# Performance work log

Measured on AMD Instinct MI355X. Metric: run time of the kernel, lower is better.

The kernel has to match this reference:

```python
import jax, jax.numpy as jnp
import numpy as np

B, R, C, D = 8, 64, 16, 128  # batch, num_rows(taxa), patch_num, embed_dim


def _linear_init(key, fan_in, fan_out):
    lim = 1.0 / np.sqrt(fan_in)
    kw, kb = jax.random.split(key)
    W = jax.random.uniform(kw, (fan_in, fan_out), jnp.float32, -lim, lim)
    b = jax.random.uniform(kb, (fan_out,), jnp.float32, -lim, lim)
    return W, b


def setup_inputs() -> dict:
    key = jax.random.key(0)
    ks = jax.random.split(key, 8)
    row_np, col_np = np.triu_indices(R, k=1)  # n = R*(R-1)/2 = 2016 pairs
    hW, hb = _linear_init(ks[1], D, D)
    gW, gb = _linear_init(ks[2], D, D)
    qW, qb = _linear_init(ks[3], D, D)
    kW, kb = _linear_init(ks[4], D, D)
    s1W, s1b = _linear_init(ks[5], D, D)
    s2W, s2b = _linear_init(ks[6], D, 1)
    return {
        "batch_input": jax.random.normal(ks[0], (B, R, C, D), jnp.float32),
        "seq_mask": jnp.ones((B, 1, C), jnp.float32),
        "row": jnp.asarray(row_np, jnp.int32),
        "col": jnp.asarray(col_np, jnp.int32),
        "hW": hW, "hb": hb, "gW": gW, "gb": gb,
        "qW": qW, "qb": qb, "kW": kW, "kb": kb,
        "s1W": s1W, "s1b": s1b, "s2W": s2W, "s2b": s2b,
    }


def reference(batch_input, seq_mask, row, col,
              hW, hb, gW, gb, qW, qb, kW, kb, s1W, s1b, s2W, s2b):
    b, r, c, d = batch_input.shape
    n = row.shape[0]
    # pairwise gather: x_i, x_j -> [b, n, c, d]
    x_i = batch_input[:, row]
    x_j = batch_input[:, col]
    # sigmoid gate fusion of the pair
    h = (x_i - x_j) @ hW + hb
    z = jax.nn.sigmoid(h)
    x = z * x_i + (1.0 - z) * x_j
    # masked global attention over the batch_input 'memory' (r > 2 branch)
    q = x @ qW + qb                    # [b, n, c, d]
    k = batch_input @ kW + kb          # [b, r, c, d]
    scale = 1.0 / np.sqrt(d * c).astype(np.float32)
    alpha = jnp.einsum('bncd,brcd->bnr', q, k) * scale
    # -inf at (pair n, rows row[n] and col[n]); equivalent to += -inf on finite scores
    neg_mask = (jnp.zeros((n, r), bool)
                .at[jnp.arange(n), row].set(True)
                .at[jnp.arange(n), col].set(True))
    alpha = jnp.where(neg_mask[None], -jnp.inf, alpha)
    alpha = jax.nn.softmax(alpha, axis=-1)
    x_glob = jnp.einsum('bnr,brcd->bncd', alpha, batch_input)
    g = x_glob @ gW + gb
    w = jax.nn.sigmoid(g)
    x = (1.0 - w) * x + w * x_glob
    # s_out: Linear -> GELU(exact) -> Linear(d,1), then mask and reduce over c
    s = jax.nn.gelu(x @ s1W + s1b, approximate=False) @ s2W + s2b  # [b, n, c, 1]
    scores = s[..., 0] * seq_mask       # seq_mask [b,1,c] broadcasts over n
    return scores.sum(-1)               # [b, n]
```

## Files before the change

kernel.cpp:

```cpp
#include <hip/hip_runtime.h>
#include <hip/hip_bf16.h>
#include <math.h>

#define B_    8
#define R_    64
#define C_    16
#define D_    128
#define NPAIR 2016
#define CD    2048
#define PG    16
#define NPG   126
#define XSTR  136
#define LSTR  68
#define NEG_BIG (-1e30f)
#define SCALE 0.022097086912079608f

typedef __attribute__((ext_vector_type(8))) short short8;
typedef __attribute__((ext_vector_type(4))) float float4v;

#define WMH  0u
#define WML  16384u
#define WSH  98304u
#define VECO 131072u
#define QBKO 131592u
#define MO   132616u
#define XTO  1181192u
#define GTO  2229768u
#define HO   3278344u

__device__ __forceinline__ unsigned short f2b(float f){
    union { float f; unsigned int u; } v; v.f = f;
    const unsigned int r = v.u + 0x7FFFu + ((v.u >> 16) & 1u);
    return (unsigned short)(r >> 16);
}
__device__ __forceinline__ float b2f(unsigned short u){
    union { unsigned int i; float f; } v; v.i = ((unsigned int)u) << 16; return v.f;
}
__device__ __forceinline__ float lo2f(unsigned int u){
    union { unsigned int i; float f; } v; v.i = u << 16; return v.f;
}
__device__ __forceinline__ float hif2f(unsigned int u){
    union { unsigned int i; float f; } v; v.i = u & 0xffff0000u; return v.f;
}
__device__ __forceinline__ unsigned int pack2(float a, float b){
    unsigned int r;
    asm("v_cvt_pk_bf16_f32 %0, %1, %2" : "=v"(r) : "v"(a), "v"(b));
    return r;
}
__device__ __forceinline__ unsigned short f2b1(float a){
    unsigned int r;
    asm("v_cvt_pk_bf16_f32 %0, %1, %1" : "=v"(r) : "v"(a));
    return (unsigned short)r;
}
__device__ __forceinline__ void split_bf(float v, float* hi, float* lo){
    union { float f; unsigned int u; } x; x.f = v;
    const unsigned int r = (x.u + 0x7FFFu + ((x.u >> 16) & 1u)) & 0xffff0000u;
    union { unsigned int u; float f; } h; h.u = r;
    *hi = h.f; *lo = v - h.f;
}
__device__ __forceinline__ void splitw(float v, short* h, short* l){
    union { float f; unsigned int u; } x; x.f = v;
    const unsigned int rh = (x.u + 0x7FFFu + ((x.u >> 16) & 1u)) & 0xffff0000u;
    union { unsigned int u; float f; } hf; hf.u = rh;
    *h = (short)(rh >> 16);
    *l = (short)f2b(v - hf.f);
}
__device__ __forceinline__ float sigmoid_safe(float x){
    return __builtin_amdgcn_rcpf(1.f + __expf(-x));
}
__device__ __forceinline__ float gelu_tanh(float x){
    const float u = x*x;
    const float g2 = x*(1.5957691216057308f + 0.07135481627159f*u);
    return x * sigmoid_safe(g2);
}

__global__ __launch_bounds__(256) void k_prepA(
    const float* __restrict__ qW, const float* __restrict__ qb,
    const float* __restrict__ kW, const float* __restrict__ kb,
    unsigned short* __restrict__ ws)
{
    const int bid = blockIdx.x, t = threadIdx.x;
    if (bid < 64){
        __shared__ float sKW[2][128];
        const int e0 = bid*2;
        sKW[t>>7][t&127] = kW[(e0 + (t>>7))*128 + (t&127)];
        __syncthreads();
        const int e = t>>7, d = t&127;
        const float* qr = qW + d*128;
        const float* kr = sKW[e];
        float acc = 0.f;
        #pragma unroll 8
        for (int g = 0; g < 128; g += 4){
            const float4 qv = *reinterpret_cast<const float4*>(qr + g);
            acc += qv.x*kr[g] + qv.y*kr[g+1] + qv.z*kr[g+2] + qv.w*kr[g+3];
        }
        float hi, lo; split_bf(acc, &hi, &lo);
        ws[WMH + d*128 + (e0+e)] = f2b(hi);
        ws[WML + d*128 + (e0+e)] = f2b(lo);
    } else {
        float* vec = (float*)(ws + VECO);
        if (t < 128){
            float a1 = 0.f, a2 = 0.f;
            #pragma unroll 8
            for (int g = 0; g < 128; g += 4){
                const float4 q4 = *reinterpret_cast<const float4*>(qW + t*128 + g);
                const float4 k4 = *reinterpret_cast<const float4*>(kW + t*128 + g);
                const float4 kb4 = *reinterpret_cast<const float4*>(kb + g);
                const float4 qb4 = *reinterpret_cast<const float4*>(qb + g);
                a1 += q4.x*kb4.x + q4.y*kb4.y + q4.z*kb4.z + q4.w*kb4.w;
                a2 += k4.x*qb4.x + k4.y*qb4.y + k4.z*qb4.z + k4.w*qb4.w;
            }
            vec[t] = a1;
            vec[128 + t] = a2;
        } else if (t == 128){
            float a = 0.f;
            for (int g = 0; g < 128; ++g) a = fmaf(qb[g], kb[g], a);
            vec[256] = a;
        }
    }
}

__global__ __launch_bounds__(512) void k_prepB(const float* __restrict__ x,
        const float* __restrict__ hW, const float* __restrict__ gW,
        const float* __restrict__ gb, const float* __restrict__ s1W,
        unsigned short* __restrict__ ws)
{
    __shared__ __align__(16) unsigned short smem[8832];
    __shared__ float sQ[4];
    const int bid = blockIdx.x, t = threadIdx.x;
    const int w = t >> 6, lane = t & 63, l15 = lane & 15, quad = lane >> 4;

    if (bid < 256){
        const bool isM = (bid >= 128);
        unsigned short* sH = smem;
        const int br0 = (bid & 127) * 4;
        const float* kqf = (const float*)(ws + VECO) + 128;
        const float* mbf = (const float*)(ws + VECO);
        if (t < 4) sQ[t] = 0.f;
        __syncthreads();
        float qacc[4] = {0.f, 0.f, 0.f, 0.f};
        #pragma unroll
        for (int i = 0; i < 4; ++i){
            const int flat = (t + 512*i)*4;
            const int lr = i;
            const int cd = flat & 2047;
            const float4 v = *reinterpret_cast<const float4*>(x + (size_t)(br0+lr)*CD + cd);
            const int ad = (lr*16 + (cd>>7))*XSTR + lr*8 + (cd & 127);
            uint2 uh;
            uh.x = pack2(v.x, v.y); uh.y = pack2(v.z, v.w);
            *reinterpret_cast<uint2*>(sH + ad) = uh;
            if (isM){
                const float4 kq4 = *reinterpret_cast<const float4*>(kqf + (cd & 127));
                qacc[i] = v.x*kq4.x + v.y*kq4.y + v.z*kq4.z + v.w*kq4.w;
            }
        }
        if (isM){
            #pragma unroll
            for (int i = 0; i < 4; ++i){
                float s = qacc[i];
                #pragma unroll
                for (int off = 1; off < 64; off <<= 1) s += __shfl_xor(s, off);
                if (lane == 0) atomicAdd(&sQ[i], s);
            }
        }
        __syncthreads();
        if (isM){
            const float bv = mbf[w*16 + l15];
            float4v acc[4];
            #pragma unroll
            for (int mt = 0; mt < 4; ++mt){ float4v d = {bv,bv,bv,bv}; acc[mt] = d; }
            #pragma unroll
            for (int ks = 0; ks < 4; ++ks){
                const int ko = ks*32 + quad*8;
                const int bd = (w*16 + l15)*128 + ko;
                const short8 bh = *reinterpret_cast<const short8*>(ws + WMH + bd);
                const short8 bl = *reinterpret_cast<const short8*>(ws + WML + bd);
                #pragma unroll
                for (int mt = 0; mt < 4; ++mt){
                    const int ad = (mt*16 + l15)*XSTR + mt*8 + ko;
                    const short8 ah = *reinterpret_cast<const short8*>(sH + ad);
                    float4v d = acc[mt];
                    d = __builtin_amdgcn_mfma_f32_16x16x32_bf16(ah, bh, d, 0,0,0);
                    d = __builtin_amdgcn_mfma_f32_16x16x32_bf16(ah, bl, d, 0,0,0);
                    acc[mt] = d;
                }
            }
            const int f = w*16 + l15;
            #pragma unroll
            for (int mt = 0; mt < 4; ++mt)
            #pragma unroll
            for (int e = 0; e < 4; ++e){
                const int c = quad*4 + e;
                ws[MO + (size_t)(br0+mt)*CD + c*128 + f] = f2b(acc[mt][e]);
            }
            if (t < 4){
                const float s0 = ((const float*)(ws + VECO))[256];
                ((float*)(ws + QBKO))[br0 + t] = sQ[t] + 16.f*s0;
            }
        } else {
            const int n = w*16 + l15;
            float4v acc[4];
            #pragma unroll
            for (int mt = 0; mt < 4; ++mt){ float4v z = {0.f,0.f,0.f,0.f}; acc[mt] = z; }
            #pragma unroll
            for (int ks = 0; ks < 4; ++ks){
                const int ko = ks*32 + quad*8;
                short8 bh, bl;
                #pragma unroll
                for (int j = 0; j < 8; ++j){
                    short hh, ll;
                    splitw(hW[(size_t)(ko+j)*128 + n], &hh, &ll);
                    bh[j] = hh; bl[j] = ll;
                }
                #pragma unroll
                for (int mt = 0; mt < 4; ++mt){
                    const int ad = (mt*16 + l15)*XSTR + mt*8 + ko;
                    const short8 ah = *reinterpret_cast<const short8*>(sH + ad);
                    float4v d = acc[mt];
                    d = __builtin_amdgcn_mfma_f32_16x16x32_bf16(ah, bh, d, 0,0,0);
                    d = __builtin_amdgcn_mfma_f32_16x16x32_bf16(ah, bl, d, 0,0,0);
                    acc[mt] = d;
                }
            }
            #pragma unroll
            for (int mt = 0; mt < 4; ++mt)
            #pragma unroll
            for (int e = 0; e < 4; ++e){
                const int c = quad*4 + e;
                ws[HO + (size_t)(br0+mt)*CD + c*128 + n] = f2b(acc[mt][e]);
            }
        }
    } else if (bid < 384){
        unsigned short* tileB = smem;
        const int gidx = bid - 256;
        const int b = gidx >> 4, cd0 = (gidx & 15)*128;
        #pragma unroll
        for (int i = 0; i < 16; ++i){
            const int idx = i*512 + t;
            const int r = idx >> 7, dd = idx & 127;
            tileB[r*138 + dd] = f2b(x[(size_t)(b*64 + r)*CD + cd0 + dd]);
        }
        __syncthreads();
        const int fA = w*16 + l15;
        float4v acc[4];
        #pragma unroll
        for (int nt = 0; nt < 4; ++nt){ float4v z = {0.f,0.f,0.f,0.f}; acc[nt] = z; }
        #pragma unroll
        for (int ks = 0; ks < 4; ++ks){
            const int ko = ks*32 + quad*8;
            short8 ah, al;
            #pragma unroll
            for (int j = 0; j < 8; ++j){
                short hh, ll;
                splitw(gW[(size_t)(ko+j)*128 + fA], &hh, &ll);
                ah[j] = hh; al[j] = ll;
            }
            #pragma unroll
            for (int nt = 0; nt < 4; ++nt){
                const short8 bb = *reinterpret_cast<const short8*>(tileB + (nt*16 + l15)*138 + ko);
                float4v d = acc[nt];
                d = __builtin_amdgcn_mfma_f32_16x16x32_bf16(ah, bb, d, 0,0,0);
                d = __builtin_amdgcn_mfma_f32_16x16x32_bf16(al, bb, d, 0,0,0);
                acc[nt] = d;
            }
        }
        #pragma unroll
        for (int nt = 0; nt < 4; ++nt)
        #pragma unroll
        for (int e = 0; e < 4; ++e){
            const int f = w*16 + quad*4 + e;
            const float val = acc[nt][e] + gb[f];
            ws[GTO + (size_t)(b*2048 + cd0 + f)*64 + nt*16 + l15] = f2b(val);
        }
    } else if (bid < 388){
        const int gid = (bid - 384)*4096 + t;
        #pragma unroll
        for (int i = 0; i < 8; ++i){
            const int g = gid + i*512;
            const int n = g >> 7, k = g & 127;
            ws[WSH + g] = f2b(s1W[k*128 + n]);
        }
    } else {
        unsigned short* tile = smem;
        const int blk = bid - 388;
        const int b = blk >> 4, cd0 = (blk & 15)*128;
        #pragma unroll
        for (int i = 0; i < 16; ++i){
            const int idx = i*512 + t;
            const int r = idx >> 7, cc = idx & 127;
            tile[cc*69 + r] = f2b(x[((size_t)(b*64 + r))*CD + cd0 + cc]);
        }
        __syncthreads();
        const unsigned int base = XTO + (unsigned int)(b*2048 + cd0)*64;
        #pragma unroll
        for (int j = 0; j < 16; ++j){
            const int idx = j*512 + t;
            const int cc = idx >> 6, r = idx & 63;
            ws[base + cc*64 + r] = tile[cc*69 + r];
        }
    }
}

__global__ __launch_bounds__(512, 4) void k_main(
    const float* __restrict__ x, const float* __restrict__ seq_mask,
    const int* __restrict__ row, const int* __restrict__ col,
    const float* __restrict__ hb, const float* __restrict__ s1b,
    const float* __restrict__ s2W, const float* __restrict__ s2b,
    const unsigned short* __restrict__ ws, float* __restrict__ out)
{
    __shared__ __align__(16) unsigned short sX[256*XSTR + 128];
    __shared__ __align__(16) unsigned short sAl[16*72];
    __shared__ float sLog[16*LSTR];
    __shared__ float sOut[PG];
    __shared__ float sMask[16];
    __shared__ int srp[PG], scp[PG];

    const int t = threadIdx.x;
    const int w = t >> 6, lane = t & 63, l15 = lane & 15, quad = lane >> 4;
    const int b = blockIdx.x, p0 = blockIdx.y * PG;
    const float* xb = x + (size_t)b * R_ * CD;
    const unsigned short* Hb = ws + HO + (size_t)b * R_ * CD;

    if (t < PG){ srp[t] = row[p0+t]; scp[t] = col[p0+t]; sOut[t] = 0.f; }
    if (t >= 32 && t < 48) sMask[t-32] = seq_mask[b*C_ + (t-32)];
    for (int i = t; i < 1152; i += 512) sAl[i] = 0;
    for (int i = t; i < 16*LSTR; i += 512) sLog[i] = 0.f;
    __syncthreads();

    #pragma unroll 4
    for (int i = 0; i < 16; ++i){
        const int flat = (t + 512*i)*4;
        const int p = flat >> 11, cd = flat & 2047;
        const int ri = srp[p], ci = scp[p];
        const float4 xi = *reinterpret_cast<const float4*>(xb + (size_t)ri*CD + cd);
        const float4 xj = *reinterpret_cast<const float4*>(xb + (size_t)ci*CD + cd);
        const uint2 Hi2 = *reinterpret_cast<const uint2*>(Hb + (size_t)ri*CD + cd);
        const uint2 Hj2 = *reinterpret_cast<const uint2*>(Hb + (size_t)ci*CD + cd);
        const float4 h4 = *reinterpret_cast<const float4*>(hb + (cd & 127));
        const float z0 = sigmoid_safe(lo2f(Hi2.x)  - lo2f(Hj2.x)  + h4.x);
        const float z1 = sigmoid_safe(hif2f(Hi2.x) - hif2f(Hj2.x) + h4.y);
        const float z2 = sigmoid_safe(lo2f(Hi2.y)  - lo2f(Hj2.y)  + h4.z);
        const float z3 = sigmoid_safe(hif2f(Hi2.y) - hif2f(Hj2.y) + h4.w);
        const float v0 = xj.x + z0*(xi.x - xj.x);
        const float v1 = xj.y + z1*(xi.y - xj.y);
        const float v2 = xj.z + z2*(xi.z - xj.z);
        const float v3 = xj.w + z3*(xi.w - xj.w);
        const int ad = (p*16 + (cd>>7))*XSTR + p*8 + (cd & 127);
        uint2 uv; uv.x = pack2(v0,v1); uv.y = pack2(v2,v3);
        *reinterpret_cast<uint2*>(sX + ad) = uv;
    }
    __syncthreads();

    {
        const int rt = w & 3, kh = w >> 2;
        const int r = rt*16 + l15;
        const unsigned short* Mr = ws + MO + ((size_t)b*64 + r)*CD + kh*1024;
        float4v d0 = {0.f,0.f,0.f,0.f}, d1 = {0.f,0.f,0.f,0.f};
        float4v d2 = {0.f,0.f,0.f,0.f}, d3 = {0.f,0.f,0.f,0.f};
        #pragma unroll
        for (int h = 0; h < 4; ++h){
            short8 bhr[8];
            #pragma unroll
            for (int u = 0; u < 8; ++u)
                bhr[u] = *reinterpret_cast<const short8*>(Mr + (h*8+u)*32 + quad*8);
            #pragma unroll
            for (int u = 0; u < 8; ++u){
                const int k = kh*1024 + (h*8+u)*32 + quad*8;
                const short8 ah = *reinterpret_cast<const short8*>(
                    sX + (l15*16 + (k>>7))*XSTR + l15*8 + (k & 127));
                if ((u&3) == 0)      d0 = __builtin_amdgcn_mfma_f32_16x16x32_bf16(ah, bhr[u], d0, 0,0,0);
                else if ((u&3) == 1) d1 = __builtin_amdgcn_mfma_f32_16x16x32_bf16(ah, bhr[u], d1, 0,0,0);
                else if ((u&3) == 2) d2 = __builtin_amdgcn_mfma_f32_16x16x32_bf16(ah, bhr[u], d2, 0,0,0);
                else                 d3 = __builtin_amdgcn_mfma_f32_16x16x32_bf16(ah, bhr[u], d3, 0,0,0);
            }
        }
        const float4v d = (d0 + d1) + (d2 + d3);
        #pragma unroll
        for (int e = 0; e < 4; ++e){
            const int pp = quad*4 + e;
            atomicAdd(&sLog[pp*LSTR + r], d[e]);
        }
    }
    __syncthreads();

    const unsigned short* XTb = ws + XTO + (size_t)b * CD * 64;
    const unsigned short* GTb = ws + GTO + (size_t)b * CD * 64;
    short8 px0[2], px1[2], pg0[2], pg1[2];
    #pragma unroll
    for (int j = 0; j < 2; ++j){
        const int cd = w*256 + j*16 + l15;
        px0[j] = *reinterpret_cast<const short8*>(XTb + (size_t)cd*64 + quad*8);
        px1[j] = *reinterpret_cast<const short8*>(XTb + (size_t)cd*64 + 32 + quad*8);
        pg0[j] = *reinterpret_cast<const short8*>(GTb + (size_t)cd*64 + quad*8);
        pg1[j] = *reinterpret_cast<const short8*>(GTb + (size_t)cd*64 + 32 + quad*8);
    }

    if (t < 256){
        const int pp = t >> 4, l = t & 15;
        const int ri = srp[pp], ci = scp[pp];
        const float* qbk = (const float*)(ws + QBKO);
        float v[4]; float m = NEG_BIG;
        #pragma unroll
        for (int k = 0; k < 4; ++k){
            const int r = l + 16*k;
            float lv = (sLog[pp*LSTR + r] + qbk[b*64 + r]) * SCALE;
            if (r == ri || r == ci) lv = NEG_BIG;
            v[k] = lv; m = fmaxf(m, lv);
        }
        #pragma unroll
        for (int s = 1; s < 16; s <<= 1) m = fmaxf(m, __shfl_xor(m, s));
        float e4[4]; float sum = 0.f;
        #pragma unroll
        for (int k = 0; k < 4; ++k){
            const int r = l + 16*k;
            const bool masked = (r == ri || r == ci);
            const float e = masked ? 0.f : __expf(fmaxf(v[k]-m, -80.f));
            e4[k] = e; sum += e;
        }
        #pragma unroll
        for (int s = 1; s < 16; s <<= 1) sum += __shfl_xor(sum, s);
        const float inv = __builtin_amdgcn_rcpf(sum);
        #pragma unroll
        for (int k = 0; k < 4; ++k) sAl[pp*72 + l + 16*k] = f2b1(e4[k]*inv);
    }
    __syncthreads();

    {
        const short8 Ah0 = *reinterpret_cast<const short8*>(sAl + l15*72 + quad*8);
        const short8 Ah1 = *reinterpret_cast<const short8*>(sAl + l15*72 + 32 + quad*8);
        #pragma unroll
        for (int j = 0; j < 16; ++j){
            const int s = j & 1;
            float4v dx = {0.f,0.f,0.f,0.f}, dg = {0.f,0.f,0.f,0.f};
            dx = __builtin_amdgcn_mfma_f32_16x16x32_bf16(Ah0, px0[s], dx, 0,0,0);
            dx = __builtin_amdgcn_mfma_f32_16x16x32_bf16(Ah1, px1[s], dx, 0,0,0);
            dg = __builtin_amdgcn_mfma_f32_16x16x32_bf16(Ah0, pg0[s], dg, 0,0,0);
            dg = __builtin_amdgcn_mfma_f32_16x16x32_bf16(Ah1, pg1[s], dg, 0,0,0);
            if (j + 2 < 16){
                const int cd2 = w*256 + (j+2)*16 + l15;
                px0[s] = *reinterpret_cast<const short8*>(XTb + (size_t)cd2*64 + quad*8);
                px1[s] = *reinterpret_cast<const short8*>(XTb + (size_t)cd2*64 + 32 + quad*8);
                pg0[s] = *reinterpret_cast<const short8*>(GTb + (size_t)cd2*64 + quad*8);
                pg1[s] = *reinterpret_cast<const short8*>(GTb + (size_t)cd2*64 + 32 + quad*8);
            }
            const int cd = w*256 + j*16 + l15;
            #pragma unroll
            for (int e = 0; e < 4; ++e){
                const int pp = quad*4 + e;
                const int ad = (pp*16 + (cd>>7))*XSTR + pp*8 + (cd & 127);
                const float wv = sigmoid_safe(dg[e]);
                const float xo = b2f(sX[ad]);
                sX[ad] = f2b1((1.f - wv)*xo + wv*dx[e]);
            }
        }
    }
    __syncthreads();

    {
        float4v acc16[16];
        const float bv = s1b[w*16 + l15];
        #pragma unroll
        for (int mt = 0; mt < 16; ++mt){ float4v d = {bv,bv,bv,bv}; acc16[mt] = d; }
        short8 bh4[4];
        #pragma unroll
        for (int ks = 0; ks < 4; ++ks)
            bh4[ks] = *reinterpret_cast<const short8*>(ws + WSH + (w*16 + l15)*128 + ks*32 + quad*8);
        #pragma unroll
        for (int ks = 0; ks < 4; ++ks){
            const int ko = ks*32 + quad*8;
            #pragma unroll
            for (int mt = 0; mt < 16; ++mt){
                const short8 a = *reinterpret_cast<const short8*>(sX + (mt*16 + l15)*XSTR + mt*8 + ko);
                acc16[mt] = __builtin_amdgcn_mfma_f32_16x16x32_bf16(a, bh4[ks], acc16[mt], 0,0,0);
            }
        }
        const float s2v = s2W[w*16 + l15];
        const float mk0 = sMask[quad*4+0], mk1 = sMask[quad*4+1];
        const float mk2 = sMask[quad*4+2], mk3 = sMask[quad*4+3];
        float psum[16];
        #pragma unroll
        for (int mt = 0; mt < 16; ++mt){
            float s = gelu_tanh(acc16[mt][0]) * mk0;
            s += gelu_tanh(acc16[mt][1]) * mk1;
            s += gelu_tanh(acc16[mt][2]) * mk2;
            s += gelu_tanh(acc16[mt][3]) * mk3;
            psum[mt] = s * s2v;
        }
        #pragma unroll
        for (int s = 1; s < 64; s <<= 1)
            #pragma unroll
            for (int mt = 0; mt < 16; ++mt) psum[mt] += __shfl_xor(psum[mt], s);
        if (lane == 0){
            #pragma unroll
            for (int mt = 0; mt < 16; ++mt) atomicAdd(&sOut[mt], psum[mt]);
        }
    }
    __syncthreads();

    if (t < PG){
        float msum = 0.f;
        #pragma unroll
        for (int c = 0; c < 16; ++c) msum += sMask[c];
        out[(size_t)b*NPAIR + p0 + t] = sOut[t] + s2b[0]*msum;
    }
}

extern "C" void kernel_launch(void* const* d_in, const int* in_sizes, int n_in,
                              void* d_out, int out_size, void* d_ws, size_t ws_size,
                              hipStream_t stream)
{
    const float* x    = (const float*)d_in[0];
    const float* mask = (const float*)d_in[1];
    const int*   row  = (const int*)d_in[2];
    const int*   col  = (const int*)d_in[3];
    const float* hW  = (const float*)d_in[4];  const float* hb  = (const float*)d_in[5];
    const float* gW  = (const float*)d_in[6];  const float* gb  = (const float*)d_in[7];
    const float* qW  = (const float*)d_in[8];  const float* qb  = (const float*)d_in[9];
    const float* kW  = (const float*)d_in[10]; const float* kb  = (const float*)d_in[11];
    const float* s1W = (const float*)d_in[12]; const float* s1b = (const float*)d_in[13];
    const float* s2W = (const float*)d_in[14]; const float* s2b = (const float*)d_in[15];

    unsigned short* ws = (unsigned short*)d_ws;

    k_prepA<<<65, 256, 0, stream>>>(qW, qb, kW, kb, ws);
    k_prepB<<<516, 512, 0, stream>>>(x, hW, gW, gb, s1W, ws);
    k_main<<<dim3(B_, NPG), 512, 0, stream>>>(x, mask, row, col,
                                              hb, s1b, s2W, s2b,
                                              ws, (float*)d_out);
}
```

Measured before the change: 227.3 us.

## Process 32 pairs per block with 1024 threads to reuse weight tiles

Doubles the pair group per block from 16 to 32 and the block size from 512 to 1024 threads, halving the grid. In the logits and global-attention stages each wave now runs two pair tiles against the same loaded M, XT and GT fragments. This cuts redundant global loads of those per-batch tiles per pair. The final s1 GEMM splits waves into two pair halves. In exchange the LDS footprint roughly doubles, so only one block fits per CU. The 1024-thread launch bound also tightens the register budget and risks spills.

```diff
diff --git a/kernel.cpp b/kernel.cpp
--- a/kernel.cpp
+++ b/kernel.cpp
@@ -8,8 +8,8 @@
 #define D_    128
 #define NPAIR 2016
 #define CD    2048
-#define PG    16
-#define NPG   126
+#define PG    32
+#define NPG   63
 #define XSTR  136
 #define LSTR  68
 #define NEG_BIG (-1e30f)
@@ -301,16 +301,16 @@
     }
 }
 
-__global__ __launch_bounds__(512, 4) void k_main(
+__global__ __launch_bounds__(1024, 4) void k_main(
     const float* __restrict__ x, const float* __restrict__ seq_mask,
     const int* __restrict__ row, const int* __restrict__ col,
     const float* __restrict__ hb, const float* __restrict__ s1b,
     const float* __restrict__ s2W, const float* __restrict__ s2b,
     const unsigned short* __restrict__ ws, float* __restrict__ out)
 {
-    __shared__ __align__(16) unsigned short sX[256*XSTR + 128];
-    __shared__ __align__(16) unsigned short sAl[16*72];
-    __shared__ float sLog[16*LSTR];
+    __shared__ __align__(16) unsigned short sX[512*XSTR + 256];
+    __shared__ __align__(16) unsigned short sAl[32*72];
+    __shared__ float sLog[32*LSTR];
     __shared__ float sOut[PG];
     __shared__ float sMask[16];
     __shared__ int srp[PG], scp[PG];
@@ -323,13 +323,13 @@
 
     if (t < PG){ srp[t] = row[p0+t]; scp[t] = col[p0+t]; sOut[t] = 0.f; }
     if (t >= 32 && t < 48) sMask[t-32] = seq_mask[b*C_ + (t-32)];
-    for (int i = t; i < 1152; i += 512) sAl[i] = 0;
-    for (int i = t; i < 16*LSTR; i += 512) sLog[i] = 0.f;
+    for (int i = t; i < 32*72; i += 1024) sAl[i] = 0;
+    for (int i = t; i < 32*LSTR; i += 1024) sLog[i] = 0.f;
     __syncthreads();
 
     #pragma unroll 4
     for (int i = 0; i < 16; ++i){
-        const int flat = (t + 512*i)*4;
+        const int flat = (t + 1024*i)*4;
         const int p = flat >> 11, cd = flat & 2047;
         const int ri = srp[p], ci = scp[p];
         const float4 xi = *reinterpret_cast<const float4*>(xb + (size_t)ri*CD + cd);
@@ -354,31 +354,40 @@
     {
         const int rt = w & 3, kh = w >> 2;
         const int r = rt*16 + l15;
-        const unsigned short* Mr = ws + MO + ((size_t)b*64 + r)*CD + kh*1024;
-        float4v d0 = {0.f,0.f,0.f,0.f}, d1 = {0.f,0.f,0.f,0.f};
-        float4v d2 = {0.f,0.f,0.f,0.f}, d3 = {0.f,0.f,0.f,0.f};
-        #pragma unroll
-        for (int h = 0; h < 4; ++h){
+        const unsigned short* Mr = ws + MO + ((size_t)b*64 + r)*CD + kh*512;
+        float4v d0a = {0.f,0.f,0.f,0.f}, d0b = {0.f,0.f,0.f,0.f};
+        float4v d1a = {0.f,0.f,0.f,0.f}, d1b = {0.f,0.f,0.f,0.f};
+        #pragma unroll
+        for (int h = 0; h < 2; ++h){
             short8 bhr[8];
             #pragma unroll
             for (int u = 0; u < 8; ++u)
                 bhr[u] = *reinterpret_cast<const short8*>(Mr + (h*8+u)*32 + quad*8);
             #pragma unroll
             for (int u = 0; u < 8; ++u){
-                const int k = kh*1024 + (h*8+u)*32 + quad*8;
-                const short8 ah = *reinterpret_cast<const short8*>(
-                    sX + (l15*16 + (k>>7))*XSTR + l15*8 + (k & 127));
-                if ((u&3) == 0)      d0 = __builtin_amdgcn_mfma_f32_16x16x32_bf16(ah, bhr[u], d0, 0,0,0);
-                else if ((u&3) == 1) d1 = __builtin_amdgcn_mfma_f32_16x16x32_bf16(ah, bhr[u], d1, 0,0,0);
-                else if ((u&3) == 2) d2 = __builtin_amdgcn_mfma_f32_16x16x32_bf16(ah, bhr[u], d2, 0,0,0);
-                else                 d3 = __builtin_amdgcn_mfma_f32_16x16x32_bf16(ah, bhr[u], d3, 0,0,0);
-            }
-        }
-        const float4v d = (d0 + d1) + (d2 + d3);
+                const int k = kh*512 + (h*8+u)*32 + quad*8;
+                const int khi = k >> 7, klo = k & 127;
+                const int pA = l15, pB = 16 + l15;
+                const short8 ahA = *reinterpret_cast<const short8*>(
+                    sX + (pA*16 + khi)*XSTR + pA*8 + klo);
+                const short8 ahB = *reinterpret_cast<const short8*>(
+                    sX + (pB*16 + khi)*XSTR + pB*8 + klo);
+                if (u & 1){
+                    d0b = __builtin_amdgcn_mfma_f32_16x16x32_bf16(ahA, bhr[u], d0b, 0,0,0);
+                    d1b = __builtin_amdgcn_mfma_f32_16x16x32_bf16(ahB, bhr[u], d1b, 0,0,0);
+                } else {
+                    d0a = __builtin_amdgcn_mfma_f32_16x16x32_bf16(ahA, bhr[u], d0a, 0,0,0);
+                    d1a = __builtin_amdgcn_mfma_f32_16x16x32_bf16(ahB, bhr[u], d1a, 0,0,0);
+                }
+            }
+        }
+        const float4v dA = d0a + d0b;
+        const float4v dB = d1a + d1b;
         #pragma unroll
         for (int e = 0; e < 4; ++e){
             const int pp = quad*4 + e;
-            atomicAdd(&sLog[pp*LSTR + r], d[e]);
+            atomicAdd(&sLog[pp*LSTR + r], dA[e]);
+            atomicAdd(&sLog[(16+pp)*LSTR + r], dB[e]);
         }
     }
     __syncthreads();
@@ -388,14 +397,14 @@
     short8 px0[2], px1[2], pg0[2], pg1[2];
     #pragma unroll
     for (int j = 0; j < 2; ++j){
-        const int cd = w*256 + j*16 + l15;
+        const int cd = w*128 + j*16 + l15;
         px0[j] = *reinterpret_cast<const short8*>(XTb + (size_t)cd*64 + quad*8);
         px1[j] = *reinterpret_cast<const short8*>(XTb + (size_t)cd*64 + 32 + quad*8);
         pg0[j] = *reinterpret_cast<const short8*>(GTb + (size_t)cd*64 + quad*8);
         pg1[j] = *reinterpret_cast<const short8*>(GTb + (size_t)cd*64 + 32 + quad*8);
     }
 
-    if (t < 256){
+    if (t < 512){
         const int pp = t >> 4, l = t & 15;
         const int ri = srp[pp], ci = scp[pp];
         const float* qbk = (const float*)(ws + QBKO);
@@ -426,55 +435,70 @@
     __syncthreads();
 
     {
-        const short8 Ah0 = *reinterpret_cast<const short8*>(sAl + l15*72 + quad*8);
-        const short8 Ah1 = *reinterpret_cast<const short8*>(sAl + l15*72 + 32 + quad*8);
-        #pragma unroll
-        for (int j = 0; j < 16; ++j){
+        const short8 AhA0 = *reinterpret_cast<const short8*>(sAl + l15*72 + quad*8);
+        const short8 AhA1 = *reinterpret_cast<const short8*>(sAl + l15*72 + 32 + quad*8);
+        const short8 AhB0 = *reinterpret_cast<const short8*>(sAl + (16+l15)*72 + quad*8);
+        const short8 AhB1 = *reinterpret_cast<const short8*>(sAl + (16+l15)*72 + 32 + quad*8);
+        #pragma unroll
+        for (int j = 0; j < 8; ++j){
             const int s = j & 1;
-            float4v dx = {0.f,0.f,0.f,0.f}, dg = {0.f,0.f,0.f,0.f};
-            dx = __builtin_amdgcn_mfma_f32_16x16x32_bf16(Ah0, px0[s], dx, 0,0,0);
-            dx = __builtin_amdgcn_mfma_f32_16x16x32_bf16(Ah1, px1[s], dx, 0,0,0);
-            dg = __builtin_amdgcn_mfma_f32_16x16x32_bf16(Ah0, pg0[s], dg, 0,0,0);
-            dg = __builtin_amdgcn_mfma_f32_16x16x32_bf16(Ah1, pg1[s], dg, 0,0,0);
-            if (j + 2 < 16){
-                const int cd2 = w*256 + (j+2)*16 + l15;
+            float4v dxA = {0.f,0.f,0.f,0.f}, dgA = {0.f,0.f,0.f,0.f};
+            float4v dxB = {0.f,0.f,0.f,0.f}, dgB = {0.f,0.f,0.f,0.f};
+            dxA = __builtin_amdgcn_mfma_f32_16x16x32_bf16(AhA0, px0[s], dxA, 0,0,0);
+            dxA = __builtin_amdgcn_mfma_f32_16x16x32_bf16(AhA1, px1[s], dxA, 0,0,0);
+            dgA = __builtin_amdgcn_mfma_f32_16x16x32_bf16(AhA0, pg0[s], dgA, 0,0,0);
+            dgA = __builtin_amdgcn_mfma_f32_16x16x32_bf16(AhA1, pg1[s], dgA, 0,0,0);
+            dxB = __builtin_amdgcn_mfma_f32_16x16x32_bf16(AhB0, px0[s], dxB, 0,0,0);
+            dxB = __builtin_amdgcn_mfma_f32_16x16x32_bf16(AhB1, px1[s], dxB, 0,0,0);
+            dgB = __builtin_amdgcn_mfma_f32_16x16x32_bf16(AhB0, pg0[s], dgB, 0,0,0);
+            dgB = __builtin_amdgcn_mfma_f32_16x16x32_bf16(AhB1, pg1[s], dgB, 0,0,0);
+            if (j + 2 < 8){
+                const int cd2 = w*128 + (j+2)*16 + l15;
                 px0[s] = *reinterpret_cast<const short8*>(XTb + (size_t)cd2*64 + quad*8);
                 px1[s] = *reinterpret_cast<const short8*>(XTb + (size_t)cd2*64 + 32 + quad*8);
                 pg0[s] = *reinterpret_cast<const short8*>(GTb + (size_t)cd2*64 + quad*8);
                 pg1[s] = *reinterpret_cast<const short8*>(GTb + (size_t)cd2*64 + 32 + quad*8);
             }
-            const int cd = w*256 + j*16 + l15;
+            const int cd = w*128 + j*16 + l15;
+            const int khi = cd >> 7, klo = cd & 127;
             #pragma unroll
             for (int e = 0; e < 4; ++e){
-                const int pp = quad*4 + e;
-                const int ad = (pp*16 + (cd>>7))*XSTR + pp*8 + (cd & 127);
-                const float wv = sigmoid_safe(dg[e]);
-                const float xo = b2f(sX[ad]);
-                sX[ad] = f2b1((1.f - wv)*xo + wv*dx[e]);
+                const int ppA = quad*4 + e;
+                const int adA = (ppA*16 + khi)*XSTR + ppA*8 + klo;
+                const float wvA = sigmoid_safe(dgA[e]);
+                const float xoA = b2f(sX[adA]);
+                sX[adA] = f2b1((1.f - wvA)*xoA + wvA*dxA[e]);
+                const int ppB = 16 + quad*4 + e;
+                const int adB = (ppB*16 + khi)*XSTR + ppB*8 + klo;
+                const float wvB = sigmoid_safe(dgB[e]);
+                const float xoB = b2f(sX[adB]);
+                sX[adB] = f2b1((1.f - wvB)*xoB + wvB*dxB[e]);
             }
         }
     }
     __syncthreads();
 
     {
+        const int mh = w >> 3, nw = w & 7;
         float4v acc16[16];
-        const float bv = s1b[w*16 + l15];
+        const float bv = s1b[nw*16 + l15];
         #pragma unroll
         for (int mt = 0; mt < 16; ++mt){ float4v d = {bv,bv,bv,bv}; acc16[mt] = d; }
         short8 bh4[4];
         #pragma unroll
         for (int ks = 0; ks < 4; ++ks)
-            bh4[ks] = *reinterpret_cast<const short8*>(ws + WSH + (w*16 + l15)*128 + ks*32 + quad*8);
+            bh4[ks] = *reinterpret_cast<const short8*>(ws + WSH + (nw*16 + l15)*128 + ks*32 + quad*8);
         #pragma unroll
         for (int ks = 0; ks < 4; ++ks){
             const int ko = ks*32 + quad*8;
             #pragma unroll
             for (int mt = 0; mt < 16; ++mt){
-                const short8 a = *reinterpret_cast<const short8*>(sX + (mt*16 + l15)*XSTR + mt*8 + ko);
+                const int p = mh*16 + mt;
+                const short8 a = *reinterpret_cast<const short8*>(sX + (p*16 + l15)*XSTR + p*8 + ko);
                 acc16[mt] = __builtin_amdgcn_mfma_f32_16x16x32_bf16(a, bh4[ks], acc16[mt], 0,0,0);
             }
         }
-        const float s2v = s2W[w*16 + l15];
+        const float s2v = s2W[nw*16 + l15];
         const float mk0 = sMask[quad*4+0], mk1 = sMask[quad*4+1];
         const float mk2 = sMask[quad*4+2], mk3 = sMask[quad*4+3];
         float psum[16];
@@ -492,7 +516,7 @@
             for (int mt = 0; mt < 16; ++mt) psum[mt] += __shfl_xor(psum[mt], s);
         if (lane == 0){
             #pragma unroll
-            for (int mt = 0; mt < 16; ++mt) atomicAdd(&sOut[mt], psum[mt]);
+            for (int mt = 0; mt < 16; ++mt) atomicAdd(&sOut[mh*16 + mt], psum[mt]);
         }
     }
     __syncthreads();
@@ -524,7 +548,7 @@
 
     k_prepA<<<65, 256, 0, stream>>>(qW, qb, kW, kb, ws);
     k_prepB<<<516, 512, 0, stream>>>(x, hW, gW, gb, s1W, ws);
-    k_main<<<dim3(B_, NPG), 512, 0, stream>>>(x, mask, row, col,
-                                              hb, s1b, s2W, s2b,
-                                              ws, (float*)d_out);
-}
+    k_main<<<dim3(B_, NPG), 1024, 0, stream>>>(x, mask, row, col,
+                                               hb, s1b, s2W, s2b,
+                                               ws, (float*)d_out);
+}
```

Result: faster. 204.7 us (-10.0%).
